# Optimization experiments

Hardware: AMD Instinct MI355X
Metric: run time of the kernel (lower is better)

## Reference

```python
import jax, jax.numpy as jnp
import numpy as np

N = 50000      # nodes
E = 800000     # edges
H, C = 4, 32   # heads, per-head channels
NF = 513       # n_fft//2 + 1 frequency bins
NMEL = 128
NEG_SLOPE_ATT = 0.2   # GATConv leaky_relu slope
NEG_SLOPE_MLP = 0.01  # F.leaky_relu default


def setup_inputs() -> dict:
    key = jax.random.key(0)
    ks = jax.random.split(key, 12)
    s = 0.05
    return {
        "x": jax.random.normal(ks[0], (N, NF), jnp.float32),
        "edge_index": jax.random.randint(ks[1], (2, E), 0, N, dtype=jnp.int32),
        "fb": jax.random.normal(ks[2], (NF, NMEL), jnp.float32) * s,
        "Wg": jax.random.normal(ks[3], (NMEL, H * C), jnp.float32) * s,
        "bias_g": jnp.zeros((H * C,), jnp.float32),
        "att_src": jax.random.normal(ks[4], (H, C), jnp.float32) * s,
        "att_dst": jax.random.normal(ks[5], (H, C), jnp.float32) * s,
        "W1": jax.random.normal(ks[6], (H * C, 256), jnp.float32) * s,
        "b1": jnp.zeros((256,), jnp.float32),
        "W2": jax.random.normal(ks[7], (256, 128), jnp.float32) * s,
        "b2": jnp.zeros((128,), jnp.float32),
        "W3": jax.random.normal(ks[8], (128, 10), jnp.float32) * s,
        "b3": jnp.zeros((10,), jnp.float32),
    }


def gat_conv(h, src, dst, att_src, att_dst, bias_g):
    # h: [N, H, C]; per-edge attention, segment softmax over dst, scatter-add
    a_s = jnp.einsum('nhc,hc->nh', h, att_src)  # [N, H]
    a_d = jnp.einsum('nhc,hc->nh', h, att_dst)  # [N, H]
    e = jax.nn.leaky_relu(a_s[src] + a_d[dst], NEG_SLOPE_ATT)  # [E', H]
    m = jax.ops.segment_max(e, dst, num_segments=N)            # [N, H]
    ex = jnp.exp(e - m[dst])
    denom = jax.ops.segment_sum(ex, dst, num_segments=N)       # [N, H]
    alpha = ex / denom[dst]                                    # [E', H]
    msg = h[src] * alpha[:, :, None]                           # [E', H, C]
    out = jax.ops.segment_sum(msg, dst, num_segments=N)        # [N, H, C]
    return out.reshape(N, H * C) + bias_g


def reference(x, edge_index, fb, Wg, bias_g, att_src, att_dst, W1, b1, W2, b2, W3, b3):
    # learnable mel filterbank projection: [N, NF] -> [N, NMEL]
    x = x @ fb
    # GATConv linear transform, split into heads
    h = (x @ Wg).reshape(N, H, C)
    # add self loops (PyG GATConv default add_self_loops=True)
    loop = jnp.arange(N, dtype=edge_index.dtype)
    src = jnp.concatenate([edge_index[0], loop])
    dst = jnp.concatenate([edge_index[1], loop])
    x = jax.nn.elu(gat_conv(h, src, dst, att_src, att_dst, bias_g))
    # dropout is identity in eval mode
    x = jax.nn.leaky_relu(x @ W1 + b1, NEG_SLOPE_MLP)
    x = jax.nn.leaky_relu(x @ W2 + b2, NEG_SLOPE_MLP)
    x = jax.nn.leaky_relu(x @ W3 + b3, NEG_SLOPE_MLP)
    return jax.nn.softmax(x, axis=-1)
```

## Files before the change

kernel.cpp:

```cpp
#include <hip/hip_runtime.h>
#include <hip/hip_bf16.h>

#define NN 50000
#define EE 800000
#define NFR 513
#define NMEL 128
#define HC 128

typedef __bf16 bf16x8 __attribute__((ext_vector_type(8)));
typedef float floatx4 __attribute__((ext_vector_type(4)));

struct __attribute__((packed, aligned(4))) u4a { unsigned x, y, z, w; };

__device__ __forceinline__ unsigned short f2b(float f) {
    unsigned u = __float_as_uint(f);
    u = (u + 0x7FFFu + ((u >> 16) & 1u)) >> 16;
    return (unsigned short)u;
}
__device__ __forceinline__ unsigned short f2bu(unsigned u) {
    u = (u + 0x7FFFu + ((u >> 16) & 1u)) >> 16;
    return (unsigned short)u;
}
__device__ __forceinline__ float b2f(unsigned short s) {
    return __uint_as_float(((unsigned)s) << 16);
}
__device__ __forceinline__ float lexp(float a) {
    a = a > 0.f ? a : 0.2f * a;
    return __expf(a);
}
__device__ __forceinline__ void stf(__hip_bfloat16* p, long i, float v) {
    ((unsigned short*)p)[i] = f2b(v);
}

__global__ __launch_bounds__(256) void k_prep(const float* __restrict__ fb, const float* __restrict__ Wg,
                                              __hip_bfloat16* __restrict__ fbWgT,
                                              const float* __restrict__ W1, __hip_bfloat16* __restrict__ W1T,
                                              const float* __restrict__ W2, __hip_bfloat16* __restrict__ W2T)
{
    const int b = blockIdx.x, t = threadIdx.x;
    if (b >= 18) {
        if (b < 146) {
            int id = (b - 18) * 256 + t;
            int n = id >> 7, k = id & 127;
            ((unsigned short*)W1T)[id] = f2b(W1[(long)k * 256 + n]);
        } else {
            int id = (b - 146) * 256 + t;
            int n = id >> 8, k = id & 255;
            ((unsigned short*)W2T)[id] = f2b(W2[(long)k * 128 + n]);
        }
        return;
    }
    __shared__ float As[16][68];
    __shared__ float Bs[16][68];
    const int row0 = (b % 9) * 64;
    const int col0 = (b / 9) * 64;
    const int tc = t & 15, tr = t >> 4;
    float acc[4][4] = {};

    for (int kb = 0; kb < NMEL; kb += 16) {
        #pragma unroll
        for (int i = 0; i < 4; ++i) {
            int idx = i * 256 + t;
            int r = idx >> 4, k = idx & 15;
            int gr = row0 + r, gk = kb + k;
            float v = 0.f;
            if (gr < NFR) v = fb[(long)gr * NMEL + gk];
            As[k][r] = v;
        }
        #pragma unroll
        for (int i = 0; i < 4; ++i) {
            int idx = i * 256 + t;
            int c = idx & 63, k = idx >> 6;
            int gk = kb + k, gc = col0 + c;
            Bs[k][c] = Wg[(long)gk * HC + gc];
        }
        __syncthreads();
        #pragma unroll
        for (int kk = 0; kk < 16; ++kk) {
            float4 av = *reinterpret_cast<const float4*>(&As[kk][tr << 2]);
            float4 bv = *reinterpret_cast<const float4*>(&Bs[kk][tc << 2]);
            float a[4] = {av.x, av.y, av.z, av.w};
            float bb[4] = {bv.x, bv.y, bv.z, bv.w};
            #pragma unroll
            for (int i = 0; i < 4; ++i)
                #pragma unroll
                for (int j = 0; j < 4; ++j)
                    acc[i][j] += a[i] * bb[j];
        }
        __syncthreads();
    }
    #pragma unroll
    for (int i = 0; i < 4; ++i) {
        int gr = row0 + (tr << 2) + i;
        if (gr >= NFR) continue;
        #pragma unroll
        for (int j = 0; j < 4; ++j) {
            int gc = col0 + (tc << 2) + j;
            ((unsigned short*)fbWgT)[(long)gc * 544 + gr] = f2b(acc[i][j]);
        }
    }
}

#define PS 40

template<typename T> struct ARegs;
template<> struct ARegs<float> { unsigned v[8]; };
template<> struct ARegs<__hip_bfloat16> { uint4 v; };

__device__ __forceinline__ void loadA_r(const float* __restrict__ A, ARegs<float>& r, int t,
                                        int row0, int M, int K, int kb)
{
    #pragma unroll
    for (int g = 0; g < 2; ++g) {
        int q = g * 256 + t;
        int row = q >> 3, k4 = (q & 7) * 4;
        int gr = row0 + row, gk = kb + k4;
        unsigned f0 = 0, f1 = 0, f2 = 0, f3 = 0;
        if (gr < M) {
            const float* ap = A + (long)gr * K + gk;
            if (gk + 3 < K) {
                u4a u = *reinterpret_cast<const u4a*>(ap);
                f0 = u.x; f1 = u.y; f2 = u.z; f3 = u.w;
            } else {
                if (gk + 0 < K) f0 = __float_as_uint(ap[0]);
                if (gk + 1 < K) f1 = __float_as_uint(ap[1]);
                if (gk + 2 < K) f2 = __float_as_uint(ap[2]);
            }
        }
        r.v[g * 4 + 0] = f0; r.v[g * 4 + 1] = f1;
        r.v[g * 4 + 2] = f2; r.v[g * 4 + 3] = f3;
    }
}

__device__ __forceinline__ void writeA_r(unsigned short* As, const ARegs<float>& r, int t)
{
    #pragma unroll
    for (int g = 0; g < 2; ++g) {
        int q = g * 256 + t;
        int row = q >> 3, k4 = (q & 7) * 4;
        ushort4 pk;
        pk.x = f2bu(r.v[g * 4 + 0]); pk.y = f2bu(r.v[g * 4 + 1]);
        pk.z = f2bu(r.v[g * 4 + 2]); pk.w = f2bu(r.v[g * 4 + 3]);
        *reinterpret_cast<ushort4*>(&As[row * PS + k4]) = pk;
    }
}

__device__ __forceinline__ void loadA_r(const __hip_bfloat16* __restrict__ A, ARegs<__hip_bfloat16>& r,
                                        int t, int row0, int M, int K, int kb)
{
    int row = t >> 2, k8 = (t & 3) * 8;
    int gr = row0 + row;
    uint4 val = make_uint4(0, 0, 0, 0);
    if (gr < M) val = *reinterpret_cast<const uint4*>(A + (long)gr * K + kb + k8);
    r.v = val;
}

__device__ __forceinline__ void writeA_r(unsigned short* As, const ARegs<__hip_bfloat16>& r, int t)
{
    int row = t >> 2, k8 = (t & 3) * 8;
    *reinterpret_cast<uint4*>(&As[row * PS + k8]) = r.v;
}

__device__ __forceinline__ void loadB_r(const __hip_bfloat16* __restrict__ Bt, uint4* bR, int t,
                                        int col0, int Nn, int KB, int kb)
{
    #pragma unroll
    for (int g = 0; g < 2; ++g) {
        int c = g * 256 + t;
        int row = c >> 2, k8 = (c & 3) * 8;
        int gn = col0 + row;
        uint4 val = make_uint4(0, 0, 0, 0);
        if (gn < Nn) val = *reinterpret_cast<const uint4*>(Bt + (long)gn * KB + kb + k8);
        bR[g] = val;
    }
}

__device__ __forceinline__ void writeB_r(unsigned short* Bs, const uint4* bR, int t)
{
    #pragma unroll
    for (int g = 0; g < 2; ++g) {
        int c = g * 256 + t;
        int row = c >> 2, k8 = (c & 3) * 8;
        *reinterpret_cast<uint4*>(&Bs[row * PS + k8]) = bR[g];
    }
}

template<int EPI, typename TA, typename TC>
__global__ __launch_bounds__(256) void mgemm(const TA* __restrict__ A,
                                             const __hip_bfloat16* __restrict__ Bt,
                                             TC* __restrict__ C,
                                             int M, int Nn, int K, int KB,
                                             const float* __restrict__ bias,
                                             const float* __restrict__ pf1,
                                             const float* __restrict__ pf2,
                                             float* __restrict__ po1,
                                             float* __restrict__ po2,
                                             const int* __restrict__ ei,
                                             int* __restrict__ hist)
{
    if (EPI == 4 && blockIdx.x >= 782) {
        int e = (blockIdx.x - 782) * 256 + (int)threadIdx.x;
        if (e < EE) atomicAdd(&hist[ei[EE + e]], 1);
        return;
    }

    __shared__ unsigned short As[2][64 * PS];
    __shared__ unsigned short Bs[2][128 * PS];

    const int t = threadIdx.x;
    const int row0 = blockIdx.x * 64;
    const int col0 = blockIdx.y * 128;
    const int wave = t >> 6, lane = t & 63;
    const int wm = (wave >> 1) * 32, wn = (wave & 1) * 64;
    const int lm = lane & 15, kq = lane >> 4;

    floatx4 acc[2][4];
    #pragma unroll
    for (int i = 0; i < 2; ++i)
        #pragma unroll
        for (int j = 0; j < 4; ++j)
            acc[i][j] = 0.f;

    ARegs<TA> aR;
    uint4 bR[2];
    loadA_r(A, aR, t, row0, M, K, 0);
    loadB_r(Bt, bR, t, col0, Nn, KB, 0);

    const int nIter = KB >> 5;
    int b = 0;
    for (int it = 0; it < nIter; ++it) {
        writeA_r(As[b], aR, t);
        writeB_r(Bs[b], bR, t);
        if (it + 1 < nIter) {
            loadA_r(A, aR, t, row0, M, K, (it + 1) * 32);
            loadB_r(Bt, bR, t, col0, Nn, KB, (it + 1) * 32);
        }
        asm volatile("s_waitcnt lgkmcnt(0)" ::: "memory");
        __builtin_amdgcn_s_barrier();
        __builtin_amdgcn_sched_barrier(0);

        bf16x8 af[2], bf[4];
        #pragma unroll
        for (int i = 0; i < 2; ++i)
            af[i] = *reinterpret_cast<const bf16x8*>(&As[b][(wm + i * 16 + lm) * PS + kq * 8]);
        #pragma unroll
        for (int j = 0; j < 4; ++j)
            bf[j] = *reinterpret_cast<const bf16x8*>(&Bs[b][(wn + j * 16 + lm) * PS + kq * 8]);
        #pragma unroll
        for (int i = 0; i < 2; ++i)
            #pragma unroll
            for (int j = 0; j < 4; ++j)
                acc[i][j] = __builtin_amdgcn_mfma_f32_16x16x32_bf16(af[i], bf[j], acc[i][j], 0, 0, 0);
        b ^= 1;
    }

    #pragma unroll
    for (int i = 0; i < 2; ++i) {
        #pragma unroll
        for (int r = 0; r < 4; ++r) {
            int gr = row0 + wm + i * 16 + kq * 4 + r;
            if (gr >= M) continue;
            #pragma unroll
            for (int j = 0; j < 4; ++j) {
                int gc = col0 + wn + j * 16 + lm;
                float v = acc[i][j][r];
                if (EPI == 1) { v += bias[gc]; v = v > 0.f ? v : 0.01f * v; }
                stf(C, (long)gr * Nn + gc, v);
            }
        }
    }

    if (EPI == 4) {
        float wsv[4], wdv[4];
        #pragma unroll
        for (int j = 0; j < 4; ++j) {
            int gc = wn + j * 16 + lm;
            wsv[j] = pf1[gc];
            wdv[j] = pf2[gc];
        }
        #pragma unroll
        for (int i = 0; i < 2; ++i) {
            #pragma unroll
            for (int r = 0; r < 4; ++r) {
                float s0 = acc[i][0][r] * wsv[0] + acc[i][1][r] * wsv[1];
                float s1 = acc[i][2][r] * wsv[2] + acc[i][3][r] * wsv[3];
                float d0 = acc[i][0][r] * wdv[0] + acc[i][1][r] * wdv[1];
                float d1 = acc[i][2][r] * wdv[2] + acc[i][3][r] * wdv[3];
                #pragma unroll
                for (int m = 1; m < 16; m <<= 1) {
                    s0 += __shfl_xor(s0, m); s1 += __shfl_xor(s1, m);
                    d0 += __shfl_xor(d0, m); d1 += __shfl_xor(d1, m);
                }
                if (lm == 0) {
                    int grow = row0 + wm + i * 16 + kq * 4 + r;
                    if (grow < M) {
                        int h0 = wn >> 5;
                        po1[grow * 4 + h0]     = s0;
                        po1[grow * 4 + h0 + 1] = s1;
                        po2[grow * 4 + h0]     = d0;
                        po2[grow * 4 + h0 + 1] = d1;
                    }
                }
            }
        }
    }
}

__global__ __launch_bounds__(512) void k_scan1(const int* __restrict__ hist, int* __restrict__ start,
                                               int* __restrict__ aux)
{
    __shared__ int sm[512];
    int t = threadIdx.x, i = blockIdx.x * 512 + t;
    int v = (i < NN) ? hist[i] : 0;
    sm[t] = v;
    __syncthreads();
    for (int off = 1; off < 512; off <<= 1) {
        int x = (t >= off) ? sm[t - off] : 0;
        __syncthreads();
        sm[t] += x;
        __syncthreads();
    }
    if (i < NN) start[i] = sm[t] - v;
    if (t == 511) aux[blockIdx.x] = sm[511];
}

__global__ void k_scan2(int* __restrict__ aux, int nb)
{
    int l = threadIdx.x;
    int v0 = (l < nb) ? aux[l] : 0;
    int v1 = (64 + l < nb) ? aux[64 + l] : 0;
    int s0 = v0, s1 = v1;
    for (int off = 1; off < 64; off <<= 1) {
        int u0 = __shfl_up(s0, off);
        int u1 = __shfl_up(s1, off);
        if (l >= off) { s0 += u0; s1 += u1; }
    }
    int tot0 = __shfl(s0, 63);
    if (l < nb) aux[l] = s0 - v0;
    if (64 + l < nb) aux[64 + l] = tot0 + s1 - v1;
}

__global__ __launch_bounds__(512) void k_scan3(int* __restrict__ start, int* __restrict__ cursor,
                                               const int* __restrict__ aux)
{
    int i = blockIdx.x * 512 + threadIdx.x;
    if (i < NN) {
        int v = start[i] + aux[blockIdx.x];
        start[i] = v;
        cursor[i] = v;
    }
    if (i == 0) start[NN] = EE;
}

__global__ void k_fill(const int* __restrict__ ei, int* __restrict__ cursor, int* __restrict__ sorted)
{
    int e = blockIdx.x * 256 + threadIdx.x;
    if (e >= EE) return;
    int s = ei[e], d = ei[EE + e];
    int pos = atomicAdd(&cursor[d], 1);
    sorted[pos] = s;
}

__global__ __launch_bounds__(256) void k_agg(const int* __restrict__ start, const int* __restrict__ sorted,
                                             const float* __restrict__ a_s, const float* __restrict__ a_d,
                                             const __hip_bfloat16* __restrict__ h,
                                             const float* __restrict__ bias_g,
                                             __hip_bfloat16* __restrict__ agg)
{
    int wave = threadIdx.x >> 6;
    int lane = threadIdx.x & 63;
    int d = blockIdx.x * 4 + wave;
    if (d >= NN) return;
    int hh = lane >> 4;
    float ad = a_d[d * 4 + hh];
    int e0 = start[d], e1 = start[d + 1];

    float ex = lexp(a_s[d * 4 + hh] + ad);
    unsigned hv = *reinterpret_cast<const unsigned*>(h + (long)d * HC + 2 * lane);
    float acc0 = ex * __uint_as_float(hv << 16);
    float acc1 = ex * __uint_as_float(hv & 0xffff0000u);
    float dsum = ex;

    int e = e0;
    for (; e + 4 <= e1; e += 4) {
        int s0 = sorted[e + 0], s1 = sorted[e + 1], s2 = sorted[e + 2], s3 = sorted[e + 3];
        float as0 = a_s[s0 * 4 + hh], as1 = a_s[s1 * 4 + hh];
        float as2 = a_s[s2 * 4 + hh], as3 = a_s[s3 * 4 + hh];
        unsigned h0 = *reinterpret_cast<const unsigned*>(h + (long)s0 * HC + 2 * lane);
        unsigned h1 = *reinterpret_cast<const unsigned*>(h + (long)s1 * HC + 2 * lane);
        unsigned h2 = *reinterpret_cast<const unsigned*>(h + (long)s2 * HC + 2 * lane);
        unsigned h3 = *reinterpret_cast<const unsigned*>(h + (long)s3 * HC + 2 * lane);
        float x0 = lexp(as0 + ad), x1 = lexp(as1 + ad), x2 = lexp(as2 + ad), x3 = lexp(as3 + ad);
        acc0 += x0 * __uint_as_float(h0 << 16);
        acc1 += x0 * __uint_as_float(h0 & 0xffff0000u);
        acc0 += x1 * __uint_as_float(h1 << 16);
        acc1 += x1 * __uint_as_float(h1 & 0xffff0000u);
        acc0 += x2 * __uint_as_float(h2 << 16);
        acc1 += x2 * __uint_as_float(h2 & 0xffff0000u);
        acc0 += x3 * __uint_as_float(h3 << 16);
        acc1 += x3 * __uint_as_float(h3 & 0xffff0000u);
        dsum += x0 + x1 + x2 + x3;
    }
    for (; e < e1; ++e) {
        int s = sorted[e];
        float xe = lexp(a_s[s * 4 + hh] + ad);
        unsigned hs = *reinterpret_cast<const unsigned*>(h + (long)s * HC + 2 * lane);
        acc0 += xe * __uint_as_float(hs << 16);
        acc1 += xe * __uint_as_float(hs & 0xffff0000u);
        dsum += xe;
    }

    float inv = 1.f / dsum;
    float2 bg = *reinterpret_cast<const float2*>(bias_g + 2 * lane);
    float v0 = acc0 * inv + bg.x;
    float v1 = acc1 * inv + bg.y;
    v0 = v0 > 0.f ? v0 : expm1f(v0);
    v1 = v1 > 0.f ? v1 : expm1f(v1);
    unsigned pk = (unsigned)f2b(v0) | ((unsigned)f2b(v1) << 16);
    *reinterpret_cast<unsigned*>((unsigned short*)agg + (long)d * HC + 2 * lane) = pk;
}

__global__ __launch_bounds__(256) void k_mlp(const __hip_bfloat16* __restrict__ A,
                                             const __hip_bfloat16* __restrict__ W1t,
                                             const __hip_bfloat16* __restrict__ W2t,
                                             const float* __restrict__ b1,
                                             const float* __restrict__ b2,
                                             const float* __restrict__ W3,
                                             const float* __restrict__ b3,
                                             float* __restrict__ out, int M)
{
    __shared__ unsigned short As[2][64 * PS];
    __shared__ unsigned short Bs[2][128 * PS];
    __shared__ unsigned short x1s[64 * 264];
    __shared__ float w3s[1280];

    const int t = threadIdx.x;
    const int row0 = blockIdx.x * 64;
    const int wave = t >> 6, lane = t & 63;
    const int wm = (wave >> 1) * 32, wn = (wave & 1) * 64;
    const int lm = lane & 15, kq = lane >> 4;

    for (int i = t; i < 1280; i += 256) w3s[i] = W3[i];

    ARegs<__hip_bfloat16> aR;
    uint4 bR[2];

    #pragma unroll 1
    for (int cp = 0; cp < 2; ++cp) {
        floatx4 acc[2][4];
        #pragma unroll
        for (int i = 0; i < 2; ++i)
            #pragma unroll
            for (int j = 0; j < 4; ++j) acc[i][j] = 0.f;

        loadA_r(A, aR, t, row0, M, 128, 0);
        loadB_r(W1t, bR, t, cp * 128, 256, 128, 0);
        int b = 0;
        #pragma unroll 1
        for (int it = 0; it < 4; ++it) {
            writeA_r(As[b], aR, t);
            writeB_r(Bs[b], bR, t);
            if (it + 1 < 4) {
                loadA_r(A, aR, t, row0, M, 128, (it + 1) * 32);
                loadB_r(W1t, bR, t, cp * 128, 256, 128, (it + 1) * 32);
            }
            asm volatile("s_waitcnt lgkmcnt(0)" ::: "memory");
            __builtin_amdgcn_s_barrier();
            __builtin_amdgcn_sched_barrier(0);

            bf16x8 af[2], bf[4];
            #pragma unroll
            for (int i = 0; i < 2; ++i)
                af[i] = *reinterpret_cast<const bf16x8*>(&As[b][(wm + i * 16 + lm) * PS + kq * 8]);
            #pragma unroll
            for (int j = 0; j < 4; ++j)
                bf[j] = *reinterpret_cast<const bf16x8*>(&Bs[b][(wn + j * 16 + lm) * PS + kq * 8]);
            #pragma unroll
            for (int i = 0; i < 2; ++i)
                #pragma unroll
                for (int j = 0; j < 4; ++j)
                    acc[i][j] = __builtin_amdgcn_mfma_f32_16x16x32_bf16(af[i], bf[j], acc[i][j], 0, 0, 0);
            b ^= 1;
        }
        #pragma unroll
        for (int i = 0; i < 2; ++i)
            #pragma unroll
            for (int r = 0; r < 4; ++r) {
                int lrow = wm + i * 16 + kq * 4 + r;
                #pragma unroll
                for (int j = 0; j < 4; ++j) {
                    int gc = cp * 128 + wn + j * 16 + lm;
                    float v = acc[i][j][r] + b1[gc];
                    v = v > 0.f ? v : 0.01f * v;
                    x1s[lrow * 264 + gc] = f2b(v);
                }
            }
    }

    loadB_r(W2t, bR, t, 0, 128, 256, 0);
    __syncthreads();

    floatx4 acc[2][4];
    #pragma unroll
    for (int i = 0; i < 2; ++i)
        #pragma unroll
        for (int j = 0; j < 4; ++j) acc[i][j] = 0.f;

    int b = 0;
    #pragma unroll 1
    for (int it = 0; it < 8; ++it) {
        writeB_r(Bs[b], bR, t);
        if (it + 1 < 8) loadB_r(W2t, bR, t, 0, 128, 256, (it + 1) * 32);
        asm volatile("s_waitcnt lgkmcnt(0)" ::: "memory");
        __builtin_amdgcn_s_barrier();
        __builtin_amdgcn_sched_barrier(0);

        bf16x8 af[2], bf[4];
        #pragma unroll
        for (int i = 0; i < 2; ++i)
            af[i] = *reinterpret_cast<const bf16x8*>(&x1s[(wm + i * 16 + lm) * 264 + it * 32 + kq * 8]);
        #pragma unroll
        for (int j = 0; j < 4; ++j)
            bf[j] = *reinterpret_cast<const bf16x8*>(&Bs[b][(wn + j * 16 + lm) * PS + kq * 8]);
        #pragma unroll
        for (int i = 0; i < 2; ++i)
            #pragma unroll
            for (int j = 0; j < 4; ++j)
                acc[i][j] = __builtin_amdgcn_mfma_f32_16x16x32_bf16(af[i], bf[j], acc[i][j], 0, 0, 0);
        b ^= 1;
    }

    __syncthreads();
    unsigned short* x2s = x1s;
    #pragma unroll
    for (int i = 0; i < 2; ++i)
        #pragma unroll
        for (int r = 0; r < 4; ++r) {
            int lrow = wm + i * 16 + kq * 4 + r;
            #pragma unroll
            for (int j = 0; j < 4; ++j) {
                int gc = wn + j * 16 + lm;
                float v = acc[i][j][r] + b2[gc];
                v = v > 0.f ? v : 0.01f * v;
                x2s[lrow * 130 + gc] = f2b(v);
            }
        }
    __syncthreads();

    if (t < 64) {
        int grow = row0 + t;
        if (grow < M) {
            float l[10];
            #pragma unroll
            for (int j = 0; j < 10; ++j) l[j] = b3[j];
            #pragma unroll 8
            for (int c = 0; c < 128; ++c) {
                float xv = b2f(x2s[t * 130 + c]);
                const float* wr = &w3s[c * 10];
                #pragma unroll
                for (int j = 0; j < 10; ++j) l[j] += xv * wr[j];
            }
            float m = -1e30f;
            #pragma unroll
            for (int j = 0; j < 10; ++j) {
                float v = l[j];
                v = v > 0.f ? v : 0.01f * v;
                l[j] = v;
                m = fmaxf(m, v);
            }
            float sum = 0.f;
            #pragma unroll
            for (int j = 0; j < 10; ++j) { l[j] = __expf(l[j] - m); sum += l[j]; }
            float inv = 1.f / sum;
            #pragma unroll
            for (int j = 0; j < 10; ++j) out[(long)grow * 10 + j] = l[j] * inv;
        }
    }
}

extern "C" void kernel_launch(void* const* d_in, const int* in_sizes, int n_in,
                              void* d_out, int out_size, void* d_ws, size_t ws_size,
                              hipStream_t stream)
{
    const float* x       = (const float*)d_in[0];
    const int*   ei      = (const int*)d_in[1];
    const float* fb      = (const float*)d_in[2];
    const float* Wg      = (const float*)d_in[3];
    const float* bias_g  = (const float*)d_in[4];
    const float* att_src = (const float*)d_in[5];
    const float* att_dst = (const float*)d_in[6];
    const float* W1      = (const float*)d_in[7];
    const float* b1      = (const float*)d_in[8];
    const float* W2      = (const float*)d_in[9];
    const float* b2      = (const float*)d_in[10];
    const float* W3      = (const float*)d_in[11];
    const float* b3      = (const float*)d_in[12];
    float* out = (float*)d_out;
    float* ws = (float*)d_ws;

    float* a_s = ws + 0;
    float* a_d = ws + 200000;
    __hip_bfloat16* fbWgT = (__hip_bfloat16*)(ws + 400000);
    __hip_bfloat16* W1T   = (__hip_bfloat16*)(ws + 434816);
    __hip_bfloat16* W2T   = (__hip_bfloat16*)(ws + 451200);
    int* hist   = (int*)(ws + 467584);
    int* startA = (int*)(ws + 517584);
    int* aux    = (int*)(ws + 567588);
    int* sorted = (int*)(ws + 567720);
    __hip_bfloat16* hbufB = (__hip_bfloat16*)(ws + 1367720);
    __hip_bfloat16* aggB  = (__hip_bfloat16*)(ws + 4567720);
    int* cursor = hist;
    if (ws_size < (size_t)14167720 * sizeof(float)) return;

    hipMemsetAsync(ws + 400000, 0, (size_t)117584 * sizeof(float), stream);

    k_prep<<<274, 256, 0, stream>>>(fb, Wg, fbWgT, W1, W1T, W2, W2T);

    mgemm<4, float, __hip_bfloat16><<<dim3(782 + (EE + 255) / 256, 1), 256, 0, stream>>>(
        x, fbWgT, hbufB, NN, HC, NFR, 544, nullptr, att_src, att_dst, a_s, a_d, ei, hist);

    k_scan1<<<98, 512, 0, stream>>>(hist, startA, aux);
    k_scan2<<<1, 64, 0, stream>>>(aux, 98);
    k_scan3<<<98, 512, 0, stream>>>(startA, cursor, aux);
    k_fill<<<(EE + 255) / 256, 256, 0, stream>>>(ei, cursor, sorted);

    k_agg<<<(NN + 3) / 4, 256, 0, stream>>>(startA, sorted, a_s, a_d, hbufB, bias_g, aggB);

    k_mlp<<<782, 256, 0, stream>>>(aggB, W1T, W2T, b1, b2, W3, b3, out, NN);
}
```

Baseline: 363.3 us.

## Fold memset into prep kernel and merge three scan kernels via last-block pattern

```diff
diff --git a/kernel.cpp b/kernel.cpp
--- a/kernel.cpp
+++ b/kernel.cpp
@@ -35,7 +35,8 @@
 __global__ __launch_bounds__(256) void k_prep(const float* __restrict__ fb, const float* __restrict__ Wg,
                                               __hip_bfloat16* __restrict__ fbWgT,
                                               const float* __restrict__ W1, __hip_bfloat16* __restrict__ W1T,
-                                              const float* __restrict__ W2, __hip_bfloat16* __restrict__ W2T)
+                                              const float* __restrict__ W2, __hip_bfloat16* __restrict__ W2T,
+                                              int* __restrict__ histz, int* __restrict__ done)
 {
     const int b = blockIdx.x, t = threadIdx.x;
     if (b >= 18) {
@@ -43,10 +44,20 @@
             int id = (b - 18) * 256 + t;
             int n = id >> 7, k = id & 127;
             ((unsigned short*)W1T)[id] = f2b(W1[(long)k * 256 + n]);
-        } else {
+        } else if (b < 274) {
             int id = (b - 146) * 256 + t;
             int n = id >> 8, k = id & 255;
             ((unsigned short*)W2T)[id] = f2b(W2[(long)k * 128 + n]);
+        } else if (b < 470) {
+            int id = (b - 274) * 256 + t;
+            if (id < NN) histz[id] = 0;
+            if (b == 274 && t == 0) *done = 0;
+        } else {
+            int id = (b - 470) * 256 + t;
+            if (id < 128 * 31) {
+                int col = id / 31, kk = 513 + id % 31;
+                ((unsigned short*)fbWgT)[(long)col * 544 + kk] = 0;
+            }
         }
         return;
     }
@@ -306,11 +317,14 @@
     }
 }
 
-__global__ __launch_bounds__(512) void k_scan1(const int* __restrict__ hist, int* __restrict__ start,
-                                               int* __restrict__ aux)
+__global__ __launch_bounds__(512) void k_scan(const int* __restrict__ hist, int* __restrict__ start,
+                                              int* __restrict__ cursor, int* __restrict__ aux,
+                                              int* __restrict__ done)
 {
     __shared__ int sm[512];
-    int t = threadIdx.x, i = blockIdx.x * 512 + t;
+    __shared__ int isLast;
+    const int t = threadIdx.x, bid = blockIdx.x;
+    int i = bid * 512 + t;
     int v = (i < NN) ? hist[i] : 0;
     sm[t] = v;
     __syncthreads();
@@ -321,35 +335,37 @@
         __syncthreads();
     }
     if (i < NN) start[i] = sm[t] - v;
-    if (t == 511) aux[blockIdx.x] = sm[511];
-}
-
-__global__ void k_scan2(int* __restrict__ aux, int nb)
-{
-    int l = threadIdx.x;
-    int v0 = (l < nb) ? aux[l] : 0;
-    int v1 = (64 + l < nb) ? aux[64 + l] : 0;
-    int s0 = v0, s1 = v1;
-    for (int off = 1; off < 64; off <<= 1) {
-        int u0 = __shfl_up(s0, off);
-        int u1 = __shfl_up(s1, off);
-        if (l >= off) { s0 += u0; s1 += u1; }
-    }
-    int tot0 = __shfl(s0, 63);
-    if (l < nb) aux[l] = s0 - v0;
-    if (64 + l < nb) aux[64 + l] = tot0 + s1 - v1;
-}
-
-__global__ __launch_bounds__(512) void k_scan3(int* __restrict__ start, int* __restrict__ cursor,
-                                               const int* __restrict__ aux)
-{
-    int i = blockIdx.x * 512 + threadIdx.x;
-    if (i < NN) {
-        int v = start[i] + aux[blockIdx.x];
-        start[i] = v;
-        cursor[i] = v;
-    }
-    if (i == 0) start[NN] = EE;
+    if (t == 511) aux[bid] = sm[511];
+
+    __threadfence();
+    __syncthreads();
+    if (t == 0) isLast = (atomicAdd(done, 1) == 97);
+    __syncthreads();
+    if (!isLast) return;
+    __threadfence();
+
+    if (t < 64) {
+        int l = t;
+        int v0 = (l < 98) ? aux[l] : 0;
+        int v1 = (64 + l < 98) ? aux[64 + l] : 0;
+        int s0 = v0, s1 = v1;
+        for (int off = 1; off < 64; off <<= 1) {
+            int u0 = __shfl_up(s0, off);
+            int u1 = __shfl_up(s1, off);
+            if (l >= off) { s0 += u0; s1 += u1; }
+        }
+        int tot0 = __shfl(s0, 63);
+        if (l < 98) aux[l] = s0 - v0;
+        if (64 + l < 98) aux[64 + l] = tot0 + s1 - v1;
+    }
+    __syncthreads();
+
+    for (int i2 = t; i2 < NN; i2 += 512) {
+        int val = start[i2] + aux[i2 >> 9];
+        start[i2] = val;
+        cursor[i2] = val;
+    }
+    if (t == 0) start[NN] = EE;
 }
 
 __global__ void k_fill(const int* __restrict__ ei, int* __restrict__ cursor, int* __restrict__ sorted)
@@ -609,19 +625,17 @@
     int* sorted = (int*)(ws + 567720);
     __hip_bfloat16* hbufB = (__hip_bfloat16*)(ws + 1367720);
     __hip_bfloat16* aggB  = (__hip_bfloat16*)(ws + 4567720);
+    int* done   = aux + 128;
     int* cursor = hist;
     if (ws_size < (size_t)14167720 * sizeof(float)) return;
 
-    hipMemsetAsync(ws + 400000, 0, (size_t)117584 * sizeof(float), stream);
-
-    k_prep<<<274, 256, 0, stream>>>(fb, Wg, fbWgT, W1, W1T, W2, W2T);
+    k_prep<<<486, 256, 0, stream>>>(fb, Wg, fbWgT, W1, W1T, W2, W2T, hist, done);
 
     mgemm<4, float, __hip_bfloat16><<<dim3(782 + (EE + 255) / 256, 1), 256, 0, stream>>>(
         x, fbWgT, hbufB, NN, HC, NFR, 544, nullptr, att_src, att_dst, a_s, a_d, ei, hist);
 
-    k_scan1<<<98, 512, 0, stream>>>(hist, startA, aux);
-    k_scan2<<<1, 64, 0, stream>>>(aux, 98);
-    k_scan3<<<98, 512, 0, stream>>>(startA, cursor, aux);
+    k_scan<<<98, 512, 0, stream>>>(hist, startA, cursor, aux, done);
+
     k_fill<<<(EE + 255) / 256, 256, 0, stream>>>(ei, cursor, sorted);
 
     k_agg<<<(NN + 3) / 4, 256, 0, stream>>>(startA, sorted, a_s, a_d, hbufB, bias_g, aggB);
```

Result: slower. 397.3 us (+9.4%).
